# Optimization experiments

Hardware: AMD Instinct MI355X
Metric: run time of the kernel (lower is better)

Reference implementation:

```python
import jax, jax.numpy as jnp
import numpy as np

NUM_EMB = 2048   # num_embeddings
TFACTOR = 4      # tokens per group (kv length)
D = 512          # embedding_dim
H = 8            # num_heads
HD = D // H      # head dim


def setup_inputs() -> dict:
    key = jax.random.key(0)
    ks = jax.random.split(key, 6)
    s = 1.0 / np.sqrt(D)
    return {
        "x": jax.random.normal(ks[0], (8, NUM_EMB * TFACTOR, D), dtype=jnp.float32),
        "pos_emb": jax.random.normal(ks[1], (TFACTOR, D), dtype=jnp.float32) * 0.02,
        "in_proj_w": jax.random.uniform(ks[2], (3 * D, D), jnp.float32, -s, s),
        "in_proj_b": jnp.zeros((3 * D,), jnp.float32),
        "out_proj_w": jax.random.uniform(ks[3], (D, D), jnp.float32, -s, s),
        "out_proj_b": jnp.zeros((D,), jnp.float32),
    }


def reference(x, pos_emb, in_proj_w, in_proj_b, out_proj_w, out_proj_b):
    B = x.shape[0]
    # group tokens: [B*NUM_EMB, TFACTOR, D]
    e = x.reshape(-1, TFACTOR, D) + pos_emb
    q = e.mean(axis=-2, keepdims=True)              # [G, 1, D]

    Wq, Wk, Wv = jnp.split(in_proj_w, 3, axis=0)
    bq, bk, bv = jnp.split(in_proj_b, 3, axis=0)

    G = e.shape[0]
    qh = (q @ Wq.T + bq).reshape(G, 1, H, HD)       # [G, 1, H, HD]
    kh = (e @ Wk.T + bk).reshape(G, TFACTOR, H, HD)
    vh = (e @ Wv.T + bv).reshape(G, TFACTOR, H, HD)

    scale = 1.0 / np.sqrt(HD)
    scores = jnp.einsum("gqhd,gkhd->ghqk", qh, kh) * scale  # [G, H, 1, TF]
    attn = jax.nn.softmax(scores, axis=-1)
    ctx = jnp.einsum("ghqk,gkhd->gqhd", attn, vh).reshape(G, 1, D)
    out = ctx @ out_proj_w.T + out_proj_b            # [G, 1, D]
    return out.reshape(B, NUM_EMB, D)
```

## Files before the change

kernel.cpp:

```cpp
#include <hip/hip_runtime.h>
#include <hip/hip_bf16.h>


#define DIM 512
#define GB 32
#define ROWS 128
#define WSZ 262144

typedef __attribute__((ext_vector_type(8))) short bf8;
typedef __attribute__((ext_vector_type(4))) float f32x4;

__device__ __forceinline__ ushort f2bs(float f) {
  union { __hip_bfloat16 b; ushort u; } c; c.b = __float2bfloat16(f); return c.u;
}
__device__ __forceinline__ float bs2f(ushort u) {
  union { unsigned int i; float f; } c; c.i = ((unsigned int)u) << 16; return c.f;
}
__device__ __forceinline__ unsigned int pack2(float a, float b) {
  return (unsigned int)f2bs(a) | ((unsigned int)f2bs(b) << 16);
}

__global__ void prep_w(const float* __restrict__ ipw, const float* __restrict__ opw,
                       ushort* __restrict__ ws) {
  int gid = blockIdx.x * 256 + threadIdx.x;
  int widx = gid >> 15;
  int rem  = gid & 32767;
  int nt   = rem >> 10;
  int ks   = (rem >> 6) & 15;
  int lane = rem & 63;
  int n  = nt * 16 + (lane & 15);
  int k0 = ks * 32 + (lane >> 4) * 8;
  const float* src;
  if      (widx == 0) src = ipw + (size_t)(512  + n) * DIM;
  else if (widx == 1) src = ipw + (size_t)(1024 + n) * DIM;
  else if (widx == 2) src = ipw + (size_t)n * DIM;
  else                src = opw + (size_t)n * DIM;
  ushort* dst = ws + (size_t)gid * 8;
#pragma unroll
  for (int j = 0; j < 8; ++j) dst[j] = f2bs(src[k0 + j]);
}

#define LDS_E   0
#define LDS_B   131072
#define LDS_TOT 163840

__device__ __forceinline__ int swz(int row, int kbyte) {
  return row * 1024 + (kbyte ^ ((row & 7) << 4));
}

__global__ __launch_bounds__(512, 2) void tdsa(
    const float* __restrict__ x, const float* __restrict__ pos,
    const float* __restrict__ ipb, const float* __restrict__ opb,
    const ushort* __restrict__ wf, float* __restrict__ out)
{
  extern __shared__ char lds[];
  const int tid  = threadIdx.x;
  const int lane = tid & 63;
  const int wave = tid >> 6;
  const int low  = lane & 15;
  const int qq   = lane >> 4;
  const int blk  = blockIdx.x;
  const size_t xbase = (size_t)blk * (ROWS * DIM);
  const int ct0 = wave * 4;

#pragma unroll
  for (int ch = 0; ch < 16; ++ch) {
    int idx = ch * 512 + tid;
    int row = idx >> 6, c8 = idx & 63;
    const float4* xp = reinterpret_cast<const float4*>(x + xbase + (size_t)row * DIM + c8 * 8);
    float4 a = xp[0], b = xp[1];
    const float4* pp = reinterpret_cast<const float4*>(pos + (row & 3) * DIM + c8 * 8);
    float4 pa = pp[0], pb = pp[1];
    uint4 u;
    u.x = pack2(a.x + pa.x, a.y + pa.y);
    u.y = pack2(a.z + pa.z, a.w + pa.w);
    u.z = pack2(b.x + pb.x, b.y + pb.y);
    u.w = pack2(b.z + pb.z, b.w + pb.w);
    *reinterpret_cast<uint4*>(&lds[LDS_E + swz(row, c8 * 16)]) = u;
  }
  __syncthreads();

#pragma unroll
  for (int ch = 0; ch < 4; ++ch) {
    int idx = ch * 512 + tid;
    int g = idx >> 6, c8 = idx & 63;
    float acc[8];
#pragma unroll
    for (int j = 0; j < 8; ++j) acc[j] = 0.f;
#pragma unroll
    for (int t = 0; t < 4; ++t) {
      bf8 v = *reinterpret_cast<const bf8*>(&lds[LDS_E + swz(g * 4 + t, c8 * 16)]);
#pragma unroll
      for (int j = 0; j < 8; ++j) acc[j] += bs2f((ushort)v[j]);
    }
    uint4 u;
    u.x = pack2(acc[0] * 0.25f, acc[1] * 0.25f);
    u.y = pack2(acc[2] * 0.25f, acc[3] * 0.25f);
    u.z = pack2(acc[4] * 0.25f, acc[5] * 0.25f);
    u.w = pack2(acc[6] * 0.25f, acc[7] * 0.25f);
    *reinterpret_cast<uint4*>(&lds[LDS_B + swz(g, c8 * 16)]) = u;
  }
  __syncthreads();

  f32x4 accK[8][4];
#pragma unroll
  for (int rt = 0; rt < 8; ++rt)
#pragma unroll
    for (int c = 0; c < 4; ++c) accK[rt][c] = (f32x4){0.f, 0.f, 0.f, 0.f};
  {
    const ushort* wk = wf;
    for (int ks = 0; ks < 16; ++ks) {
      int kbyte = ks * 64 + qq * 16;
      bf8 a[8];
#pragma unroll
      for (int rt = 0; rt < 8; ++rt)
        a[rt] = *reinterpret_cast<const bf8*>(&lds[LDS_E + swz(rt * 16 + low, kbyte)]);
      bf8 bk_[4];
#pragma unroll
      for (int c = 0; c < 4; ++c) {
        size_t fo = ((size_t)((ct0 + c) * 16 + ks) * 64 + lane) * 8;
        bk_[c] = *reinterpret_cast<const bf8*>(wk + fo);
      }
#pragma unroll
      for (int c = 0; c < 4; ++c)
#pragma unroll
        for (int rt = 0; rt < 8; ++rt)
          accK[rt][c] = __builtin_amdgcn_mfma_f32_16x16x32_bf16(a[rt], bk_[c], accK[rt][c], 0, 0, 0);
    }
  }

  f32x4 accQ[2][4];
#pragma unroll
  for (int rt = 0; rt < 2; ++rt)
#pragma unroll
    for (int c = 0; c < 4; ++c) accQ[rt][c] = (f32x4){0.f, 0.f, 0.f, 0.f};
  {
    const ushort* wq = wf + 2 * (size_t)WSZ;
    for (int ks = 0; ks < 16; ++ks) {
      int kbyte = ks * 64 + qq * 16;
      bf8 aq[2];
#pragma unroll
      for (int rt = 0; rt < 2; ++rt)
        aq[rt] = *reinterpret_cast<const bf8*>(&lds[LDS_B + swz(rt * 16 + low, kbyte)]);
      bf8 bq_[4];
#pragma unroll
      for (int c = 0; c < 4; ++c) {
        size_t fo = ((size_t)((ct0 + c) * 16 + ks) * 64 + lane) * 8;
        bq_[c] = *reinterpret_cast<const bf8*>(wq + fo);
      }
#pragma unroll
      for (int c = 0; c < 4; ++c)
#pragma unroll
        for (int rt = 0; rt < 2; ++rt)
          accQ[rt][c] = __builtin_amdgcn_mfma_f32_16x16x32_bf16(aq[rt], bq_[c], accQ[rt][c], 0, 0, 0);
    }
  }
  __syncthreads();

#pragma unroll
  for (int rtq = 0; rtq < 2; ++rtq)
#pragma unroll
    for (int c = 0; c < 4; ++c) {
      int colLocal = c * 16 + low;
#pragma unroll
      for (int j = 0; j < 4; ++j) {
        int addr = LDS_B + wave * 4096 + colLocal * 64 + j * 16 + (rtq * 4 + qq) * 2;
        *reinterpret_cast<ushort*>(&lds[addr]) = f2bs(accQ[rtq][c][j]);
      }
    }

  float sp[8][4];
#pragma unroll
  for (int rt = 0; rt < 8; ++rt)
#pragma unroll
    for (int j = 0; j < 4; ++j) sp[rt][j] = 0.f;
#pragma unroll
  for (int c = 0; c < 4; ++c) {
    int colLocal = c * 16 + low;
    bf8 qv = *reinterpret_cast<const bf8*>(&lds[LDS_B + wave * 4096 + colLocal * 64 + qq * 16]);
#pragma unroll
    for (int rt = 0; rt < 8; ++rt) {
      float qf = bs2f((ushort)qv[rt]);
#pragma unroll
      for (int j = 0; j < 4; ++j) sp[rt][j] += accK[rt][c][j] * qf;
    }
  }
#pragma unroll
  for (int mask = 1; mask <= 8; mask <<= 1)
#pragma unroll
    for (int rt = 0; rt < 8; ++rt)
#pragma unroll
      for (int j = 0; j < 4; ++j) sp[rt][j] += __shfl_xor(sp[rt][j], mask);
  float attn[8][4];
#pragma unroll
  for (int rt = 0; rt < 8; ++rt) {
    float s0 = sp[rt][0] * 0.125f, s1 = sp[rt][1] * 0.125f;
    float s2 = sp[rt][2] * 0.125f, s3 = sp[rt][3] * 0.125f;
    float m = fmaxf(fmaxf(s0, s1), fmaxf(s2, s3));
    float p0 = __expf(s0 - m), p1 = __expf(s1 - m);
    float p2 = __expf(s2 - m), p3 = __expf(s3 - m);
    float r = 1.f / (p0 + p1 + p2 + p3);
    attn[rt][0] = p0 * r; attn[rt][1] = p1 * r;
    attn[rt][2] = p2 * r; attn[rt][3] = p3 * r;
  }
  __syncthreads();

  f32x4 accV[8][4];
#pragma unroll
  for (int rt = 0; rt < 8; ++rt)
#pragma unroll
    for (int c = 0; c < 4; ++c) accV[rt][c] = (f32x4){0.f, 0.f, 0.f, 0.f};
  {
    const ushort* wv = wf + (size_t)WSZ;
    for (int ks = 0; ks < 16; ++ks) {
      int kbyte = ks * 64 + qq * 16;
      bf8 a[8];
#pragma unroll
      for (int rt = 0; rt < 8; ++rt)
        a[rt] = *reinterpret_cast<const bf8*>(&lds[LDS_E + swz(rt * 16 + low, kbyte)]);
      bf8 bv_[4];
#pragma unroll
      for (int c = 0; c < 4; ++c) {
        size_t fo = ((size_t)((ct0 + c) * 16 + ks) * 64 + lane) * 8;
        bv_[c] = *reinterpret_cast<const bf8*>(wv + fo);
      }
#pragma unroll
      for (int c = 0; c < 4; ++c)
#pragma unroll
        for (int rt = 0; rt < 8; ++rt)
          accV[rt][c] = __builtin_amdgcn_mfma_f32_16x16x32_bf16(a[rt], bv_[c], accV[rt][c], 0, 0, 0);
    }
  }

  float vb[4];
#pragma unroll
  for (int c = 0; c < 4; ++c) vb[c] = ipb[1024 + (ct0 + c) * 16 + low];
#pragma unroll
  for (int rt = 0; rt < 8; ++rt)
#pragma unroll
    for (int c = 0; c < 4; ++c) {
      float ctx = vb[c]
                + attn[rt][0] * accV[rt][c][0] + attn[rt][1] * accV[rt][c][1]
                + attn[rt][2] * accV[rt][c][2] + attn[rt][3] * accV[rt][c][3];
      int g = rt * 4 + qq;
      int col2 = ((ct0 + c) * 16 + low) * 2;
      *reinterpret_cast<ushort*>(&lds[LDS_B + g * 1024 + (col2 ^ ((g & 7) << 4))]) = f2bs(ctx);
    }
  __syncthreads();

  f32x4 accO[2][4];
#pragma unroll
  for (int rt = 0; rt < 2; ++rt)
#pragma unroll
    for (int c = 0; c < 4; ++c) accO[rt][c] = (f32x4){0.f, 0.f, 0.f, 0.f};
  {
    const ushort* wo = wf + 3 * (size_t)WSZ;
    for (int ks = 0; ks < 16; ++ks) {
      int kbyte = ks * 64 + qq * 16;
      bf8 aO[2];
#pragma unroll
      for (int rt = 0; rt < 2; ++rt)
        aO[rt] = *reinterpret_cast<const bf8*>(&lds[LDS_B + swz(rt * 16 + low, kbyte)]);
      bf8 bo_[4];
#pragma unroll
      for (int c = 0; c < 4; ++c) {
        size_t fo = ((size_t)((ct0 + c) * 16 + ks) * 64 + lane) * 8;
        bo_[c] = *reinterpret_cast<const bf8*>(wo + fo);
      }
#pragma unroll
      for (int c = 0; c < 4; ++c)
#pragma unroll
        for (int rt = 0; rt < 2; ++rt)
          accO[rt][c] = __builtin_amdgcn_mfma_f32_16x16x32_bf16(aO[rt], bo_[c], accO[rt][c], 0, 0, 0);
    }
  }
#pragma unroll
  for (int c = 0; c < 4; ++c) {
    int col = (ct0 + c) * 16 + low;
    float ob = opb[col];
#pragma unroll
    for (int rt = 0; rt < 2; ++rt)
#pragma unroll
      for (int j = 0; j < 4; ++j) {
        int g = rt * 16 + qq * 4 + j;
        out[((size_t)blk * GB + g) * DIM + col] = accO[rt][c][j] + ob;
      }
  }
}

extern "C" void kernel_launch(void* const* d_in, const int* in_sizes, int n_in,
                              void* d_out, int out_size, void* d_ws, size_t ws_size,
                              hipStream_t stream) {
  const float* x   = (const float*)d_in[0];
  const float* pos = (const float*)d_in[1];
  const float* ipw = (const float*)d_in[2];
  const float* ipb = (const float*)d_in[3];
  const float* opw = (const float*)d_in[4];
  const float* opb = (const float*)d_in[5];
  ushort* wsf = (ushort*)d_ws;

  prep_w<<<512, 256, 0, stream>>>(ipw, opw, wsf);

  hipFuncSetAttribute(reinterpret_cast<const void*>(tdsa),
                      hipFuncAttributeMaxDynamicSharedMemorySize, LDS_TOT);
  tdsa<<<512, 512, LDS_TOT, stream>>>(x, pos, ipb, opb, wsf, (float*)d_out);
}
```

Measured before the change: 390.9 us.

## Repack LDS into MFMA fragment order and split K/V projections into column halves

Stores the embedded tokens and the per-group vectors in shared memory in MFMA fragment order, so each lane reads its operand at a contiguous slot with an XOR swizzle per k-step. The Q projection now runs before K, which lets the K and V projections each be done in two passes of two column tiles, folding each pass into the score and context accumulation straight away. This halves the live accumulator registers. Launch bounds change from two blocks per CU to one, giving each thread more registers at the cost of occupancy, and the A-fragment LDS reads are repeated for each pass.

```diff
diff --git a/kernel.cpp b/kernel.cpp
--- a/kernel.cpp
+++ b/kernel.cpp
@@ -4,7 +4,6 @@
 
 #define DIM 512
 #define GB 32
-#define ROWS 128
 #define WSZ 262144
 
 typedef __attribute__((ext_vector_type(8))) short bf8;
@@ -44,11 +43,14 @@
 #define LDS_B   131072
 #define LDS_TOT 163840
 
-__device__ __forceinline__ int swz(int row, int kbyte) {
-  return row * 1024 + (kbyte ^ ((row & 7) << 4));
-}
-
-__global__ __launch_bounds__(512, 2) void tdsa(
+__device__ __forceinline__ int eaddr(int ks, int rt, int slot) {
+  return LDS_E + ((((ks << 3) + rt) << 6) + (slot ^ (ks & 7))) * 16;
+}
+__device__ __forceinline__ int baddr(int ks, int rt, int slot) {
+  return LDS_B + ((((ks << 1) + rt) << 6) + (slot ^ (ks & 7))) * 16;
+}
+
+__global__ __launch_bounds__(512, 1) void tdsa(
     const float* __restrict__ x, const float* __restrict__ pos,
     const float* __restrict__ ipb, const float* __restrict__ opb,
     const ushort* __restrict__ wf, float* __restrict__ out)
@@ -60,7 +62,7 @@
   const int low  = lane & 15;
   const int qq   = lane >> 4;
   const int blk  = blockIdx.x;
-  const size_t xbase = (size_t)blk * (ROWS * DIM);
+  const size_t xbase = (size_t)blk * (128 * DIM);
   const int ct0 = wave * 4;
 
 #pragma unroll
@@ -76,20 +78,23 @@
     u.y = pack2(a.z + pa.z, a.w + pa.w);
     u.z = pack2(b.x + pb.x, b.y + pb.y);
     u.w = pack2(b.z + pb.z, b.w + pb.w);
-    *reinterpret_cast<uint4*>(&lds[LDS_E + swz(row, c8 * 16)]) = u;
+    int ks = c8 >> 2, q8 = c8 & 3;
+    *reinterpret_cast<uint4*>(&lds[eaddr(ks, row >> 4, q8 * 16 + (row & 15))]) = u;
   }
   __syncthreads();
 
 #pragma unroll
   for (int ch = 0; ch < 4; ++ch) {
     int idx = ch * 512 + tid;
-    int g = idx >> 6, c8 = idx & 63;
+    int g = idx & 31, c8 = idx >> 5;
+    int ks = c8 >> 2, q8 = c8 & 3;
     float acc[8];
 #pragma unroll
     for (int j = 0; j < 8; ++j) acc[j] = 0.f;
 #pragma unroll
     for (int t = 0; t < 4; ++t) {
-      bf8 v = *reinterpret_cast<const bf8*>(&lds[LDS_E + swz(g * 4 + t, c8 * 16)]);
+      int r = g * 4 + t;
+      bf8 v = *reinterpret_cast<const bf8*>(&lds[eaddr(ks, r >> 4, q8 * 16 + (r & 15))]);
 #pragma unroll
       for (int j = 0; j < 8; ++j) acc[j] += bs2f((ushort)v[j]);
     }
@@ -98,36 +103,9 @@
     u.y = pack2(acc[2] * 0.25f, acc[3] * 0.25f);
     u.z = pack2(acc[4] * 0.25f, acc[5] * 0.25f);
     u.w = pack2(acc[6] * 0.25f, acc[7] * 0.25f);
-    *reinterpret_cast<uint4*>(&lds[LDS_B + swz(g, c8 * 16)]) = u;
-  }
-  __syncthreads();
-
-  f32x4 accK[8][4];
-#pragma unroll
-  for (int rt = 0; rt < 8; ++rt)
-#pragma unroll
-    for (int c = 0; c < 4; ++c) accK[rt][c] = (f32x4){0.f, 0.f, 0.f, 0.f};
-  {
-    const ushort* wk = wf;
-    for (int ks = 0; ks < 16; ++ks) {
-      int kbyte = ks * 64 + qq * 16;
-      bf8 a[8];
-#pragma unroll
-      for (int rt = 0; rt < 8; ++rt)
-        a[rt] = *reinterpret_cast<const bf8*>(&lds[LDS_E + swz(rt * 16 + low, kbyte)]);
-      bf8 bk_[4];
-#pragma unroll
-      for (int c = 0; c < 4; ++c) {
-        size_t fo = ((size_t)((ct0 + c) * 16 + ks) * 64 + lane) * 8;
-        bk_[c] = *reinterpret_cast<const bf8*>(wk + fo);
-      }
-#pragma unroll
-      for (int c = 0; c < 4; ++c)
-#pragma unroll
-        for (int rt = 0; rt < 8; ++rt)
-          accK[rt][c] = __builtin_amdgcn_mfma_f32_16x16x32_bf16(a[rt], bk_[c], accK[rt][c], 0, 0, 0);
-    }
-  }
+    *reinterpret_cast<uint4*>(&lds[baddr(ks, g >> 4, q8 * 16 + (g & 15))]) = u;
+  }
+  __syncthreads();
 
   f32x4 accQ[2][4];
 #pragma unroll
@@ -137,11 +115,10 @@
   {
     const ushort* wq = wf + 2 * (size_t)WSZ;
     for (int ks = 0; ks < 16; ++ks) {
-      int kbyte = ks * 64 + qq * 16;
       bf8 aq[2];
 #pragma unroll
       for (int rt = 0; rt < 2; ++rt)
-        aq[rt] = *reinterpret_cast<const bf8*>(&lds[LDS_B + swz(rt * 16 + low, kbyte)]);
+        aq[rt] = *reinterpret_cast<const bf8*>(&lds[baddr(ks, rt, lane)]);
       bf8 bq_[4];
 #pragma unroll
       for (int c = 0; c < 4; ++c) {
@@ -174,15 +151,44 @@
   for (int rt = 0; rt < 8; ++rt)
 #pragma unroll
     for (int j = 0; j < 4; ++j) sp[rt][j] = 0.f;
-#pragma unroll
-  for (int c = 0; c < 4; ++c) {
-    int colLocal = c * 16 + low;
-    bf8 qv = *reinterpret_cast<const bf8*>(&lds[LDS_B + wave * 4096 + colLocal * 64 + qq * 16]);
-#pragma unroll
-    for (int rt = 0; rt < 8; ++rt) {
-      float qf = bs2f((ushort)qv[rt]);
-#pragma unroll
-      for (int j = 0; j < 4; ++j) sp[rt][j] += accK[rt][c][j] * qf;
+  {
+    const ushort* wk = wf;
+    for (int c2 = 0; c2 < 2; ++c2) {
+      f32x4 accK[8][2];
+#pragma unroll
+      for (int rt = 0; rt < 8; ++rt)
+#pragma unroll
+        for (int cc = 0; cc < 2; ++cc) accK[rt][cc] = (f32x4){0.f, 0.f, 0.f, 0.f};
+      for (int ks = 0; ks < 16; ++ks) {
+        bf8 a[8];
+#pragma unroll
+        for (int rt = 0; rt < 8; ++rt)
+          a[rt] = *reinterpret_cast<const bf8*>(&lds[eaddr(ks, rt, lane)]);
+        bf8 bk_[2];
+#pragma unroll
+        for (int cc = 0; cc < 2; ++cc) {
+          int c = c2 * 2 + cc;
+          size_t fo = ((size_t)((ct0 + c) * 16 + ks) * 64 + lane) * 8;
+          bk_[cc] = *reinterpret_cast<const bf8*>(wk + fo);
+        }
+#pragma unroll
+        for (int cc = 0; cc < 2; ++cc)
+#pragma unroll
+          for (int rt = 0; rt < 8; ++rt)
+            accK[rt][cc] = __builtin_amdgcn_mfma_f32_16x16x32_bf16(a[rt], bk_[cc], accK[rt][cc], 0, 0, 0);
+      }
+#pragma unroll
+      for (int cc = 0; cc < 2; ++cc) {
+        int c = c2 * 2 + cc;
+        int colLocal = c * 16 + low;
+        bf8 qv = *reinterpret_cast<const bf8*>(&lds[LDS_B + wave * 4096 + colLocal * 64 + qq * 16]);
+#pragma unroll
+        for (int rt = 0; rt < 8; ++rt) {
+          float qf = bs2f((ushort)qv[rt]);
+#pragma unroll
+          for (int j = 0; j < 4; ++j) sp[rt][j] += accK[rt][cc][j] * qf;
+        }
+      }
     }
   }
 #pragma unroll
@@ -205,47 +211,52 @@
   }
   __syncthreads();
 
-  f32x4 accV[8][4];
-#pragma unroll
-  for (int rt = 0; rt < 8; ++rt)
-#pragma unroll
-    for (int c = 0; c < 4; ++c) accV[rt][c] = (f32x4){0.f, 0.f, 0.f, 0.f};
+  float vb[4];
+#pragma unroll
+  for (int c = 0; c < 4; ++c) vb[c] = ipb[1024 + (ct0 + c) * 16 + low];
   {
     const ushort* wv = wf + (size_t)WSZ;
-    for (int ks = 0; ks < 16; ++ks) {
-      int kbyte = ks * 64 + qq * 16;
-      bf8 a[8];
+    for (int c2 = 0; c2 < 2; ++c2) {
+      f32x4 accV[8][2];
 #pragma unroll
       for (int rt = 0; rt < 8; ++rt)
-        a[rt] = *reinterpret_cast<const bf8*>(&lds[LDS_E + swz(rt * 16 + low, kbyte)]);
-      bf8 bv_[4];
-#pragma unroll
-      for (int c = 0; c < 4; ++c) {
-        size_t fo = ((size_t)((ct0 + c) * 16 + ks) * 64 + lane) * 8;
-        bv_[c] = *reinterpret_cast<const bf8*>(wv + fo);
-      }
-#pragma unroll
-      for (int c = 0; c < 4; ++c)
+#pragma unroll
+        for (int cc = 0; cc < 2; ++cc) accV[rt][cc] = (f32x4){0.f, 0.f, 0.f, 0.f};
+      for (int ks = 0; ks < 16; ++ks) {
+        bf8 a[8];
 #pragma unroll
         for (int rt = 0; rt < 8; ++rt)
-          accV[rt][c] = __builtin_amdgcn_mfma_f32_16x16x32_bf16(a[rt], bv_[c], accV[rt][c], 0, 0, 0);
-    }
-  }
-
-  float vb[4];
-#pragma unroll
-  for (int c = 0; c < 4; ++c) vb[c] = ipb[1024 + (ct0 + c) * 16 + low];
-#pragma unroll
-  for (int rt = 0; rt < 8; ++rt)
-#pragma unroll
-    for (int c = 0; c < 4; ++c) {
-      float ctx = vb[c]
-                + attn[rt][0] * accV[rt][c][0] + attn[rt][1] * accV[rt][c][1]
-                + attn[rt][2] * accV[rt][c][2] + attn[rt][3] * accV[rt][c][3];
-      int g = rt * 4 + qq;
-      int col2 = ((ct0 + c) * 16 + low) * 2;
-      *reinterpret_cast<ushort*>(&lds[LDS_B + g * 1024 + (col2 ^ ((g & 7) << 4))]) = f2bs(ctx);
-    }
+          a[rt] = *reinterpret_cast<const bf8*>(&lds[eaddr(ks, rt, lane)]);
+        bf8 bv_[2];
+#pragma unroll
+        for (int cc = 0; cc < 2; ++cc) {
+          int c = c2 * 2 + cc;
+          size_t fo = ((size_t)((ct0 + c) * 16 + ks) * 64 + lane) * 8;
+          bv_[cc] = *reinterpret_cast<const bf8*>(wv + fo);
+        }
+#pragma unroll
+        for (int cc = 0; cc < 2; ++cc)
+#pragma unroll
+          for (int rt = 0; rt < 8; ++rt)
+            accV[rt][cc] = __builtin_amdgcn_mfma_f32_16x16x32_bf16(a[rt], bv_[cc], accV[rt][cc], 0, 0, 0);
+      }
+#pragma unroll
+      for (int cc = 0; cc < 2; ++cc) {
+        int c = c2 * 2 + cc;
+        int d = ct0 * 16 + c * 16 + low;
+        int ksd = d >> 5, qqd = (d >> 3) & 3, jd = d & 7;
+#pragma unroll
+        for (int rt = 0; rt < 8; ++rt) {
+          float ctx = vb[c]
+                    + attn[rt][0] * accV[rt][cc][0] + attn[rt][1] * accV[rt][cc][1]
+                    + attn[rt][2] * accV[rt][cc][2] + attn[rt][3] * accV[rt][cc][3];
+          int g = rt * 4 + qq;
+          int chunk = baddr(ksd, g >> 4, qqd * 16 + (g & 15));
+          *reinterpret_cast<ushort*>(&lds[chunk + jd * 2]) = f2bs(ctx);
+        }
+      }
+    }
+  }
   __syncthreads();
 
   f32x4 accO[2][4];
@@ -256,11 +267,10 @@
   {
     const ushort* wo = wf + 3 * (size_t)WSZ;
     for (int ks = 0; ks < 16; ++ks) {
-      int kbyte = ks * 64 + qq * 16;
       bf8 aO[2];
 #pragma unroll
       for (int rt = 0; rt < 2; ++rt)
-        aO[rt] = *reinterpret_cast<const bf8*>(&lds[LDS_B + swz(rt * 16 + low, kbyte)]);
+        aO[rt] = *reinterpret_cast<const bf8*>(&lds[baddr(ks, rt, lane)]);
       bf8 bo_[4];
 #pragma unroll
       for (int c = 0; c < 4; ++c) {
```

New measurement: 420.7 us. 1.08x slower.
